# Kernel tuning notes

Hardware: AMD Instinct MI355X
Metric: run time of the kernel (lower is better)

Reference implementation:

```python
import jax, jax.numpy as jnp
import numpy as np

G = 8      # num_codebooks
D = 64     # codebook_dim
V = 1024   # codebook_size
BETA = 1.0


def setup_inputs() -> dict:
    key = jax.random.key(0)
    k1, k2, k3 = jax.random.split(key, 3)
    inputs = jax.random.normal(k1, (8, 2048, G * D), dtype=jnp.float32)
    paddings = jax.random.randint(k2, (8, 2048), 0, 2, dtype=jnp.int32)
    codebook = jax.random.normal(k3, (V, G, D), dtype=jnp.float32)
    return {"inputs": inputs, "paddings": paddings, "codebook": codebook}


def reference(inputs, paddings, codebook):
    B, T, _ = inputs.shape
    x = inputs.reshape(B, T, G, D)

    # Per-group L2 nearest neighbor: dist[b,t,g,v] = ||x - c||^2
    # ||x||^2 is constant over v, drop it for the argmin.
    dots = jnp.einsum("btgd,vgd->btgv", x, codebook)          # [B,T,G,V]
    c_sq = jnp.sum(codebook * codebook, axis=-1)                # [V,G]
    dists = c_sq.T[None, None] - 2.0 * dots                     # [B,T,G,V]
    ids = jnp.argmin(dists, axis=-1)                            # [B,T,G]

    # Gather selected codes per group.
    quantized = codebook[ids, jnp.arange(G)[None, None, :]]     # [B,T,G,D]

    mask = (1.0 - paddings.astype(jnp.float32))[:, :, None, None]  # [B,T,1,1]
    denom = mask.sum()
    xd = jax.lax.stop_gradient(x)
    qd = jax.lax.stop_gradient(quantized)
    kmeans_loss = jnp.sum((quantized - xd) ** 2 * mask) / denom
    commitment_loss = jnp.sum((x - qd) ** 2 * mask) / denom
    total_loss = kmeans_loss + BETA * commitment_loss

    # Straight-through estimator, masked.
    quantized_st = (x + jax.lax.stop_gradient(quantized - x)) * mask
    quantized_st = quantized_st.reshape(B, T, G * D)

    ids = jnp.where(mask[:, :, :, 0] == 0.0, -1, ids)           # [B,T,G]
    return ids, quantized_st, kmeans_loss, commitment_loss, total_loss
```

## Files before the change

kernel.cpp:

```cpp
#include <hip/hip_runtime.h>
#include <cfloat>
#include <stdint.h>

#define G_ 8
#define D_ 64
#define V_ 1024
#define BT_ 16384
#define TPB_ 256
#define NSLOT_ 128
#define TOKS_ 128
#define NC_ 128
#define NCHUNK_ (V_ / NC_)

typedef unsigned long long u64;
typedef uint32_t u32;
typedef _Float16 h8 __attribute__((ext_vector_type(8)));
typedef _Float16 h4 __attribute__((ext_vector_type(4)));
typedef float f32x4 __attribute__((ext_vector_type(4)));

typedef __attribute__((address_space(3))) uint32_t lds_u32;
typedef __attribute__((address_space(1))) uint32_t glb_u32;

#define GL2LDS(gsrc, ldst) \
    __builtin_amdgcn_global_load_lds((glb_u32*)(gsrc), (lds_u32*)(ldst), 16, 0, 0)


__global__ void prep_csq(const float* __restrict__ cb, const int* __restrict__ pad,
                         float* __restrict__ csqT,
                         int* __restrict__ cnt, int* __restrict__ list,
                         float* __restrict__ out_ids, float* __restrict__ out_q,
                         _Float16* __restrict__ cbH, _Float16* __restrict__ cbL) {
    const int tid = threadIdx.x;
    const int idx = blockIdx.x * TPB_ + tid;

    if (idx < V_ * G_) {
        const float4* r = (const float4*)(cb + (size_t)idx * D_);
        _Float16* hp = cbH + (size_t)idx * 64;
        _Float16* lp = cbL + (size_t)idx * 64;
        float s = 0.f;
#pragma unroll
        for (int i = 0; i < D_ / 4; ++i) {
            float4 c = r[i];
            s += c.x * c.x + c.y * c.y + c.z * c.z + c.w * c.w;
            float xs[4] = {c.x, c.y, c.z, c.w};
            h4 hv, lv;
#pragma unroll
            for (int e = 0; e < 4; ++e) {
                _Float16 hh = (_Float16)xs[e];
                hv[e] = hh;
                lv[e] = (_Float16)((xs[e] - (float)hh) * 4096.f);
            }
            *(h4*)(hp + i * 4) = hv;
            *(h4*)(lp + i * 4) = lv;
        }
        csqT[(idx & (G_ - 1)) * V_ + (idx >> 3)] = s;
    }

    __shared__ int s_cnt[8];
    __shared__ int s_base, s_npl;
    __shared__ int s_plist[TPB_];
    const int lane = tid & 63, w = tid >> 6;
    const bool active = (pad[idx] == 0);
    u64 bal = __ballot(active);
    int na  = __popcll(bal);
    if (lane == 0) { s_cnt[w] = na; s_cnt[4 + w] = 64 - na; }
    __syncthreads();
    if (tid == 0) {
        int ta = s_cnt[0] + s_cnt[1] + s_cnt[2] + s_cnt[3];
        s_base = atomicAdd(cnt, ta);
        s_npl  = TPB_ - ta;
    }
    __syncthreads();
    int pre_a = 0, pre_p = 0;
    for (int i = 0; i < w; ++i) { pre_a += s_cnt[i]; pre_p += s_cnt[4 + i]; }
    const u64 mb = ((u64)1 << lane) - 1;
    if (active) list[s_base + pre_a + __popcll(bal & mb)] = idx;
    else        s_plist[pre_p + __popcll(~bal & mb)] = idx;
    __syncthreads();

    const int npl = s_npl;
    for (int i = w; i < npl; i += 4) {
        int tok = s_plist[i];
        float4 z = make_float4(0.f, 0.f, 0.f, 0.f);
        float4* q = (float4*)(out_q + (size_t)tok * (G_ * D_)) + lane * 2;
        q[0] = z;
        q[1] = z;
        if (lane < G_) out_ids[(size_t)tok * G_ + lane] = -1.0f;
    }
}

__global__ __launch_bounds__(TPB_, 2) void vq_scan(
    const float* __restrict__ inp,
    const float* __restrict__ cb,
    const float* __restrict__ csqT,
    const int* __restrict__ cnt,
    const int* __restrict__ list,
    const _Float16* __restrict__ cbH,
    const _Float16* __restrict__ cbL,
    float* __restrict__ out_ids,
    float* __restrict__ out_q,
    float* __restrict__ part) {

    __shared__ __align__(16) unsigned char BH[2][NC_ * 128];
    __shared__ __align__(16) unsigned char BL[2][NC_ * 128];
    __shared__ float csq_s[V_];
    __shared__ u64 merge_s[2][TOKS_];

    const int nact = cnt[0];
    const int tile = blockIdx.x;
    if (tile * TOKS_ >= nact) return;
    const int g   = blockIdx.y;
    const int tid = threadIdx.x;
    const int lane = tid & 63;
    const int w    = tid >> 6;
    const int mh   = w >> 1;
    const int nh   = w & 1;
    const int r16  = lane & 15;
    const int kq   = lane >> 4;

#pragma unroll
    for (int k = 0; k < 4; ++k)
        csq_s[k * 256 + tid] = csqT[g * V_ + k * 256 + tid];

    const size_t srcoff = (size_t)(w * 32 + (lane >> 3)) * 1024 + (size_t)g * 128
                        + (size_t)(((lane & 7) ^ (lane >> 3)) * 16);
    const unsigned char* sH = (const unsigned char*)cbH + srcoff;
    const unsigned char* sL = (const unsigned char*)cbL + srcoff;
    const int ldsb = w * 4096;

#pragma unroll
    for (int i = 0; i < 4; ++i) GL2LDS(sH + i * 8192, &BH[0][ldsb + i * 1024]);
#pragma unroll
    for (int i = 0; i < 4; ++i) GL2LDS(sL + i * 8192, &BL[0][ldsb + i * 1024]);

    h8 AH[4][2], AL[4][2];
#pragma unroll
    for (int rf = 0; rf < 4; ++rf) {
        int p = tile * TOKS_ + mh * 64 + rf * 16 + r16;
        int tok = list[p < nact ? p : 0];
        const float* xr = inp + (size_t)tok * (G_ * D_) + g * D_;
#pragma unroll
        for (int kf = 0; kf < 2; ++kf) {
            const float4* xp = (const float4*)(xr + kf * 32 + kq * 8);
            float4 a = xp[0], b = xp[1];
            float xs[8] = {a.x, a.y, a.z, a.w, b.x, b.y, b.z, b.w};
#pragma unroll
            for (int e = 0; e < 8; ++e) {
                _Float16 hh = (_Float16)xs[e];
                AH[rf][kf][e] = hh;
                AL[rf][kf][e] = (_Float16)((xs[e] - (float)hh) * 4096.f);
            }
        }
    }

    float bestd[16];
    int   bestid[16];
#pragma unroll
    for (int s = 0; s < 16; ++s) { bestd[s] = FLT_MAX; bestid[s] = 0; }

    __syncthreads();

    const u32 swB = (u32)((r16 & 7) << 4);
    const u32 boB = (u32)((nh * 64 + r16) * 128 + kq * 16);

    for (int c = 0; c < NCHUNK_; ++c) {
        const int cur = c & 1;
        const unsigned char* BHc = &BH[0][0] + cur * (NC_ * 128);
        const unsigned char* BLc = &BL[0][0] + cur * (NC_ * 128);

        if (c < NCHUNK_ - 1) {
            unsigned char* dH = &BH[0][0] + (cur ^ 1) * (NC_ * 128) + ldsb;
            unsigned char* dL = &BL[0][0] + (cur ^ 1) * (NC_ * 128) + ldsb;
            const unsigned char* nH = sH + (size_t)(c + 1) * 131072;
            const unsigned char* nL = sL + (size_t)(c + 1) * 131072;
#pragma unroll
            for (int i = 0; i < 4; ++i) GL2LDS(nH + i * 8192, dH + i * 1024);
#pragma unroll
            for (int i = 0; i < 4; ++i) GL2LDS(nL + i * 8192, dL + i * 1024);
        }

#pragma unroll 1
        for (int cf = 0; cf < 4; ++cf) {
            const u32 ob = boB + (u32)(cf * 2048);
            const h8 bh0 = *(const h8*)(BHc + ((ob)      ^ swB));
            const h8 bh1 = *(const h8*)(BHc + ((ob + 64) ^ swB));
            const h8 bl0 = *(const h8*)(BLc + ((ob)      ^ swB));
            const h8 bl1 = *(const h8*)(BLc + ((ob + 64) ^ swB));
            const int vcol = c * NC_ + nh * 64 + cf * 16 + r16;
            const float cq = csq_s[vcol];
#pragma unroll
            for (int rf = 0; rf < 4; ++rf) {
                f32x4 a  = {0.f, 0.f, 0.f, 0.f};
                f32x4 ac = {0.f, 0.f, 0.f, 0.f};
                a  = __builtin_amdgcn_mfma_f32_16x16x32_f16(AH[rf][0], bh0, a,  0, 0, 0);
                a  = __builtin_amdgcn_mfma_f32_16x16x32_f16(AH[rf][1], bh1, a,  0, 0, 0);
                ac = __builtin_amdgcn_mfma_f32_16x16x32_f16(AH[rf][0], bl0, ac, 0, 0, 0);
                ac = __builtin_amdgcn_mfma_f32_16x16x32_f16(AH[rf][1], bl1, ac, 0, 0, 0);
                ac = __builtin_amdgcn_mfma_f32_16x16x32_f16(AL[rf][0], bh0, ac, 0, 0, 0);
                ac = __builtin_amdgcn_mfma_f32_16x16x32_f16(AL[rf][1], bh1, ac, 0, 0, 0);
#pragma unroll
                for (int q = 0; q < 4; ++q) {
                    float d = fmaf(-2.f, a[q], cq);
                    d = fmaf(-0x1.0p-11f, ac[q], d);
                    int s = rf * 4 + q;
                    if (d < bestd[s]) { bestd[s] = d; bestid[s] = vcol; }
                }
            }
        }
        __syncthreads();
    }

#pragma unroll
    for (int s = 0; s < 16; ++s) {
        u32 u = __float_as_uint(bestd[s]);
        u = u ^ ((u >> 31) ? 0xFFFFFFFFu : 0x80000000u);
        u64 pk = ((u64)u << 32) | (u32)bestid[s];
#pragma unroll
        for (int off = 1; off <= 8; off <<= 1) {
            u64 o = __shfl_xor(pk, off, 64);
            pk = (o < pk) ? o : pk;
        }
        if (r16 == 0) {
            int row = mh * 64 + (s >> 2) * 16 + kq * 4 + (s & 3);
            merge_s[nh][row] = pk;
        }
    }
    __syncthreads();

    float l = 0.f;
    {
        int tl = tid >> 1, qv = tid & 1;
        int p  = tile * TOKS_ + tl;
        if (p < nact) {
            int tok = list[p];
            u64 qa = merge_s[0][tl], qb = merge_s[1][tl];
            u64 qm = (qb < qa) ? qb : qa;
            int id  = (int)(qm & 0xFFFFFFFFull);
            const float4* cr = (const float4*)(cb + ((size_t)id * G_ + g) * D_) + qv * 8;
            const float4* xr = (const float4*)(inp + (size_t)tok * (G_ * D_) + g * D_) + qv * 8;
            float4* qo = (float4*)(out_q + (size_t)tok * (G_ * D_) + g * D_) + qv * 8;
#pragma unroll
            for (int k = 0; k < 8; ++k) {
                float4 cc = cr[k], xx = xr[k];
                float dx = cc.x - xx.x, dy = cc.y - xx.y;
                float dz = cc.z - xx.z, dw = cc.w - xx.w;
                l += dx * dx + dy * dy + dz * dz + dw * dw;
                qo[k] = cc;
            }
            if (qv == 0) out_ids[(size_t)tok * G_ + g] = (float)id;
        }
    }
#pragma unroll
    for (int off = 32; off > 0; off >>= 1) l += __shfl_down(l, off, 64);
    if (lane == 0) {
        int slot = ((blockIdx.y * gridDim.x + blockIdx.x) * 4 + w) & (NSLOT_ - 1);
        atomicAdd(&part[slot], l);
    }
}

__global__ void finalize_kernel(const float* __restrict__ part,
                                const int* __restrict__ cnt,
                                float* __restrict__ out_losses) {
    int lane = threadIdx.x;
    float l = part[lane] + part[lane + 64];
#pragma unroll
    for (int off = 32; off > 0; off >>= 1) l += __shfl_down(l, off, 64);
    if (lane == 0) {
        float k = l / (float)cnt[0];
        out_losses[0] = k;
        out_losses[1] = k;
        out_losses[2] = 2.f * k;
    }
}

extern "C" void kernel_launch(void* const* d_in, const int* in_sizes, int n_in,
                              void* d_out, int out_size, void* d_ws, size_t ws_size,
                              hipStream_t stream) {
    const float* inp = (const float*)d_in[0];
    const int*   pad = (const int*)d_in[1];
    const float* cb  = (const float*)d_in[2];

    float* out   = (float*)d_out;
    float* o_ids = out;
    float* o_q   = out + (size_t)BT_ * G_;
    float* o_ls  = o_q + (size_t)BT_ * G_ * D_;

    float*     part = (float*)d_ws;
    int*       cnt  = (int*)((char*)d_ws + 512);
    float*     csqT = (float*)((char*)d_ws + 1024);
    int*       list = (int*)((char*)d_ws + 33792);
    _Float16*  cbH  = (_Float16*)((char*)d_ws + 131072);
    _Float16*  cbL  = (_Float16*)((char*)d_ws + 131072 + 1048576);

    hipMemsetAsync(d_ws, 0, 1024, stream);

    prep_csq<<<dim3(BT_ / TPB_), dim3(TPB_), 0, stream>>>(
        cb, pad, csqT, cnt, list, o_ids, o_q, cbH, cbL);

    dim3 grid(BT_ / TOKS_, G_);
    vq_scan<<<grid, dim3(TPB_), 0, stream>>>(
        inp, cb, csqT, cnt, list, cbH, cbL, o_ids, o_q, part);

    finalize_kernel<<<1, dim3(64), 0, stream>>>(part, cnt, o_ls);
}
```

Measured before the change: 135.3 us.

## Use 512-thread scan blocks with fewer rows per wave and fold csq into MFMA init

Doubles vq_scan block size to 8 waves, so each wave handles 32 token rows instead of 64. This halves the per-thread A fragments and running best arrays and raises the launch bound to 4 blocks per CU, aiming for more resident waves to hide latency. The distance is now computed as a max-score by seeding the MFMA accumulator with -0.5*csq, which removes per-element FMAs from the inner loop. The codebook tile copy into LDS is redistributed across the 8 waves. The trade-offs are more waves contending for shared B-tile LDS reads and tighter per-thread register limits.

```diff
diff --git a/kernel.cpp b/kernel.cpp
--- a/kernel.cpp
+++ b/kernel.cpp
@@ -6,7 +6,8 @@
 #define D_ 64
 #define V_ 1024
 #define BT_ 16384
-#define TPB_ 256
+#define TPB_ 512
+#define PREPB_ 256
 #define NSLOT_ 128
 #define TOKS_ 128
 #define NC_ 128
@@ -31,7 +32,7 @@
                          float* __restrict__ out_ids, float* __restrict__ out_q,
                          _Float16* __restrict__ cbH, _Float16* __restrict__ cbL) {
     const int tid = threadIdx.x;
-    const int idx = blockIdx.x * TPB_ + tid;
+    const int idx = blockIdx.x * PREPB_ + tid;
 
     if (idx < V_ * G_) {
         const float4* r = (const float4*)(cb + (size_t)idx * D_);
@@ -58,7 +59,7 @@
 
     __shared__ int s_cnt[8];
     __shared__ int s_base, s_npl;
-    __shared__ int s_plist[TPB_];
+    __shared__ int s_plist[PREPB_];
     const int lane = tid & 63, w = tid >> 6;
     const bool active = (pad[idx] == 0);
     u64 bal = __ballot(active);
@@ -68,7 +69,7 @@
     if (tid == 0) {
         int ta = s_cnt[0] + s_cnt[1] + s_cnt[2] + s_cnt[3];
         s_base = atomicAdd(cnt, ta);
-        s_npl  = TPB_ - ta;
+        s_npl  = PREPB_ - ta;
     }
     __syncthreads();
     int pre_a = 0, pre_p = 0;
@@ -89,7 +90,7 @@
     }
 }
 
-__global__ __launch_bounds__(TPB_, 2) void vq_scan(
+__global__ __launch_bounds__(TPB_, 4) void vq_scan(
     const float* __restrict__ inp,
     const float* __restrict__ cb,
     const float* __restrict__ csqT,
@@ -109,8 +110,8 @@
     const int nact = cnt[0];
     const int tile = blockIdx.x;
     if (tile * TOKS_ >= nact) return;
-    const int g   = blockIdx.y;
-    const int tid = threadIdx.x;
+    const int g    = blockIdx.y;
+    const int tid  = threadIdx.x;
     const int lane = tid & 63;
     const int w    = tid >> 6;
     const int mh   = w >> 1;
@@ -118,25 +119,25 @@
     const int r16  = lane & 15;
     const int kq   = lane >> 4;
 
-#pragma unroll
-    for (int k = 0; k < 4; ++k)
-        csq_s[k * 256 + tid] = csqT[g * V_ + k * 256 + tid];
-
-    const size_t srcoff = (size_t)(w * 32 + (lane >> 3)) * 1024 + (size_t)g * 128
-                        + (size_t)(((lane & 7) ^ (lane >> 3)) * 16);
-    const unsigned char* sH = (const unsigned char*)cbH + srcoff;
-    const unsigned char* sL = (const unsigned char*)cbL + srcoff;
-    const int ldsb = w * 4096;
-
-#pragma unroll
-    for (int i = 0; i < 4; ++i) GL2LDS(sH + i * 8192, &BH[0][ldsb + i * 1024]);
-#pragma unroll
-    for (int i = 0; i < 4; ++i) GL2LDS(sL + i * 8192, &BL[0][ldsb + i * 1024]);
-
-    h8 AH[4][2], AL[4][2];
-#pragma unroll
-    for (int rf = 0; rf < 4; ++rf) {
-        int p = tile * TOKS_ + mh * 64 + rf * 16 + r16;
+    const size_t soff = (size_t)(w * 8 + (lane >> 3)) * 1024
+                      + (size_t)g * 128
+                      + (size_t)(((lane & 7) ^ (lane >> 3)) * 16);
+    const unsigned char* sH = (const unsigned char*)cbH + soff;
+    const unsigned char* sL = (const unsigned char*)cbL + soff;
+    const int ldsb = w * 1024;
+
+    GL2LDS(sH,         &BH[0][ldsb]);
+    GL2LDS(sH + 65536, &BH[0][ldsb + 8192]);
+    GL2LDS(sL,         &BL[0][ldsb]);
+    GL2LDS(sL + 65536, &BL[0][ldsb + 8192]);
+
+    csq_s[tid]       = csqT[g * V_ + tid];
+    csq_s[tid + 512] = csqT[g * V_ + tid + 512];
+
+    h8 AH[2][2], AL[2][2];
+#pragma unroll
+    for (int rf = 0; rf < 2; ++rf) {
+        int p = tile * TOKS_ + mh * 32 + rf * 16 + r16;
         int tok = list[p < nact ? p : 0];
         const float* xr = inp + (size_t)tok * (G_ * D_) + g * D_;
 #pragma unroll
@@ -153,44 +154,44 @@
         }
     }
 
-    float bestd[16];
-    int   bestid[16];
-#pragma unroll
-    for (int s = 0; s < 16; ++s) { bestd[s] = FLT_MAX; bestid[s] = 0; }
-
-    __syncthreads();
-
-    const u32 swB = (u32)((r16 & 7) << 4);
-    const u32 boB = (u32)((nh * 64 + r16) * 128 + kq * 16);
+    float beste[8];
+    int   bestid[8];
+#pragma unroll
+    for (int s = 0; s < 8; ++s) { beste[s] = -FLT_MAX / 2; bestid[s] = 0; }
+
+    __syncthreads();
+
+    const u32 o0 = (u32)((((nh * 64 + r16) * 128 + kq * 16))
+                         ^ ((u32)(r16 & 7) << 4));
 
     for (int c = 0; c < NCHUNK_; ++c) {
         const int cur = c & 1;
-        const unsigned char* BHc = &BH[0][0] + cur * (NC_ * 128);
-        const unsigned char* BLc = &BL[0][0] + cur * (NC_ * 128);
+        const unsigned char* BHc = &BH[cur][0];
+        const unsigned char* BLc = &BL[cur][0];
 
         if (c < NCHUNK_ - 1) {
-            unsigned char* dH = &BH[0][0] + (cur ^ 1) * (NC_ * 128) + ldsb;
-            unsigned char* dL = &BL[0][0] + (cur ^ 1) * (NC_ * 128) + ldsb;
+            unsigned char* dH = &BH[cur ^ 1][ldsb];
+            unsigned char* dL = &BL[cur ^ 1][ldsb];
             const unsigned char* nH = sH + (size_t)(c + 1) * 131072;
             const unsigned char* nL = sL + (size_t)(c + 1) * 131072;
-#pragma unroll
-            for (int i = 0; i < 4; ++i) GL2LDS(nH + i * 8192, dH + i * 1024);
-#pragma unroll
-            for (int i = 0; i < 4; ++i) GL2LDS(nL + i * 8192, dL + i * 1024);
+            GL2LDS(nH,         dH);
+            GL2LDS(nH + 65536, dH + 8192);
+            GL2LDS(nL,         dL);
+            GL2LDS(nL + 65536, dL + 8192);
         }
 
 #pragma unroll 1
         for (int cf = 0; cf < 4; ++cf) {
-            const u32 ob = boB + (u32)(cf * 2048);
-            const h8 bh0 = *(const h8*)(BHc + ((ob)      ^ swB));
-            const h8 bh1 = *(const h8*)(BHc + ((ob + 64) ^ swB));
-            const h8 bl0 = *(const h8*)(BLc + ((ob)      ^ swB));
-            const h8 bl1 = *(const h8*)(BLc + ((ob + 64) ^ swB));
+            const u32 ob = o0 + (u32)(cf * 2048);
+            const h8 bh0 = *(const h8*)(BHc + ob);
+            const h8 bh1 = *(const h8*)(BHc + (ob ^ 64));
+            const h8 bl0 = *(const h8*)(BLc + ob);
+            const h8 bl1 = *(const h8*)(BLc + (ob ^ 64));
             const int vcol = c * NC_ + nh * 64 + cf * 16 + r16;
-            const float cq = csq_s[vcol];
-#pragma unroll
-            for (int rf = 0; rf < 4; ++rf) {
-                f32x4 a  = {0.f, 0.f, 0.f, 0.f};
+            const float ai = -0.5f * csq_s[vcol];
+#pragma unroll
+            for (int rf = 0; rf < 2; ++rf) {
+                f32x4 a  = {ai, ai, ai, ai};
                 f32x4 ac = {0.f, 0.f, 0.f, 0.f};
                 a  = __builtin_amdgcn_mfma_f32_16x16x32_f16(AH[rf][0], bh0, a,  0, 0, 0);
                 a  = __builtin_amdgcn_mfma_f32_16x16x32_f16(AH[rf][1], bh1, a,  0, 0, 0);
@@ -200,10 +201,9 @@
                 ac = __builtin_amdgcn_mfma_f32_16x16x32_f16(AL[rf][1], bh1, ac, 0, 0, 0);
 #pragma unroll
                 for (int q = 0; q < 4; ++q) {
-                    float d = fmaf(-2.f, a[q], cq);
-                    d = fmaf(-0x1.0p-11f, ac[q], d);
+                    float e = fmaf(0x1.0p-12f, ac[q], a[q]);
                     int s = rf * 4 + q;
-                    if (d < bestd[s]) { bestd[s] = d; bestid[s] = vcol; }
+                    if (e > beste[s]) { beste[s] = e; bestid[s] = vcol; }
                 }
             }
         }
@@ -211,8 +211,9 @@
     }
 
 #pragma unroll
-    for (int s = 0; s < 16; ++s) {
-        u32 u = __float_as_uint(bestd[s]);
+    for (int s = 0; s < 8; ++s) {
+        float d = -2.f * beste[s];
+        u32 u = __float_as_uint(d);
         u = u ^ ((u >> 31) ? 0xFFFFFFFFu : 0x80000000u);
         u64 pk = ((u64)u << 32) | (u32)bestid[s];
 #pragma unroll
@@ -221,7 +222,7 @@
             pk = (o < pk) ? o : pk;
         }
         if (r16 == 0) {
-            int row = mh * 64 + (s >> 2) * 16 + kq * 4 + (s & 3);
+            int row = mh * 32 + (s >> 2) * 16 + kq * 4 + (s & 3);
             merge_s[nh][row] = pk;
         }
     }
@@ -229,18 +230,18 @@
 
     float l = 0.f;
     {
-        int tl = tid >> 1, qv = tid & 1;
+        int tl = tid >> 2, qv = tid & 3;
         int p  = tile * TOKS_ + tl;
         if (p < nact) {
             int tok = list[p];
             u64 qa = merge_s[0][tl], qb = merge_s[1][tl];
             u64 qm = (qb < qa) ? qb : qa;
             int id  = (int)(qm & 0xFFFFFFFFull);
-            const float4* cr = (const float4*)(cb + ((size_t)id * G_ + g) * D_) + qv * 8;
-            const float4* xr = (const float4*)(inp + (size_t)tok * (G_ * D_) + g * D_) + qv * 8;
-            float4* qo = (float4*)(out_q + (size_t)tok * (G_ * D_) + g * D_) + qv * 8;
-#pragma unroll
-            for (int k = 0; k < 8; ++k) {
+            const float4* cr = (const float4*)(cb + ((size_t)id * G_ + g) * D_) + qv * 4;
+            const float4* xr = (const float4*)(inp + (size_t)tok * (G_ * D_) + g * D_) + qv * 4;
+            float4* qo = (float4*)(out_q + (size_t)tok * (G_ * D_) + g * D_) + qv * 4;
+#pragma unroll
+            for (int k = 0; k < 4; ++k) {
                 float4 cc = cr[k], xx = xr[k];
                 float dx = cc.x - xx.x, dy = cc.y - xx.y;
                 float dz = cc.z - xx.z, dw = cc.w - xx.w;
@@ -253,7 +254,7 @@
 #pragma unroll
     for (int off = 32; off > 0; off >>= 1) l += __shfl_down(l, off, 64);
     if (lane == 0) {
-        int slot = ((blockIdx.y * gridDim.x + blockIdx.x) * 4 + w) & (NSLOT_ - 1);
+        int slot = ((blockIdx.y * gridDim.x + blockIdx.x) * 8 + w) & (NSLOT_ - 1);
         atomicAdd(&part[slot], l);
     }
 }
@@ -294,7 +295,7 @@
 
     hipMemsetAsync(d_ws, 0, 1024, stream);
 
-    prep_csq<<<dim3(BT_ / TPB_), dim3(TPB_), 0, stream>>>(
+    prep_csq<<<dim3(BT_ / PREPB_), dim3(PREPB_), 0, stream>>>(
         cb, pad, csqT, cnt, list, o_ids, o_q, cbH, cbL);
 
     dim3 grid(BT_ / TOKS_, G_);
```

New measurement: 138.7 us. +2.5%, slower.
